# Kernel optimization log

Measured on AMD Instinct MI355X. Metric: run time of the kernel, lower is better.

The kernel has to match this reference:

```python
import jax, jax.numpy as jnp
import numpy as np

N_NODES = 50000
N_EDGES = 800000
IN_DIM = 128
HID_DIM = 128


def setup_inputs() -> dict:
    key = jax.random.key(0)
    k1, k2, k3, k4 = jax.random.split(key, 4)
    x = jax.random.normal(k1, (N_NODES, IN_DIM), dtype=jnp.float32)
    src = jax.random.randint(k2, (N_EDGES,), 0, N_NODES, dtype=jnp.int64)
    dst = jax.random.randint(k3, (N_EDGES,), 0, N_NODES, dtype=jnp.int64)
    W = jax.random.normal(k4, (IN_DIM, HID_DIM), dtype=jnp.float32) * (1.0 / np.sqrt(IN_DIM))
    b = jnp.zeros((HID_DIM,), dtype=jnp.float32)
    return {"x": x, "src": src, "dst": dst, "W": W, "b": b}


def reference(x, src, dst, W, b):
    # DGL GraphConv, norm='both': out = D_in^{-1/2} A D_out^{-1/2} x W + b
    n = x.shape[0]
    ones = jnp.ones((src.shape[0],), dtype=x.dtype)
    deg_out = jax.ops.segment_sum(ones, src, num_segments=n)  # out-degree of src side
    deg_in = jax.ops.segment_sum(ones, dst, num_segments=n)   # in-degree of dst side
    norm_src = jnp.clip(deg_out, 1.0, None) ** -0.5           # [N]
    norm_dst = jnp.clip(deg_in, 1.0, None) ** -0.5            # [N]
    h = x * norm_src[:, None]                                 # [N, in_dim]
    agg = jax.ops.segment_sum(h[src], dst, num_segments=n)    # SpMM: sum messages at dst
    agg = agg * norm_dst[:, None]
    return agg @ W + b
```

## Files before the change

### kernel.cpp

```cpp
#include <hip/hip_runtime.h>
#include <hip/hip_bf16.h>

#define DIM   128
#define BM    64
#define HALF_NODES 25088
#define HALF_PAIRS (HALF_NODES / 2)
#define FULL_PAIRS (2 * HALF_PAIRS)

typedef short  bf16x8 __attribute__((ext_vector_type(8)));
typedef float  f32x4  __attribute__((ext_vector_type(4)));

__device__ __forceinline__ ushort f2bf(float f) {
    uint u = __float_as_uint(f);
    return (ushort)((u + 0x7FFFu + ((u >> 16) & 1u)) >> 16);
}

__global__ __launch_bounds__(256) void cvtw_kernel(const float* __restrict__ W,
                                                   ushort* __restrict__ WT) {
    int idx = blockIdx.x * 256 + threadIdx.x;
    if (idx < DIM * DIM) {
        int k = idx >> 7, c = idx & 127;
        WT[c * DIM + k] = f2bf(W[idx]);
    }
}

__global__ __launch_bounds__(1024) void hist_kernel(const int* __restrict__ src,
                                                    const int* __restrict__ dst,
                                                    uint* __restrict__ histD,
                                                    uint* __restrict__ histS,
                                                    int* __restrict__ rank,
                                                    int n_edges, int pairs_row,
                                                    int nhalves, int chunk) {
    __shared__ uint h[FULL_PAIRS];
    const int c   = blockIdx.x;
    const int tid = threadIdx.x;
    const int beg = c * chunk;
    const int end = min(beg + chunk, n_edges);
    for (int pass = 0; pass < 2; ++pass) {
        const int* key = pass ? src : dst;
        uint* outb     = pass ? histS : histD;
        for (int hbase = 0; hbase < nhalves; hbase += 2) {
            const int plo    = hbase * HALF_PAIRS;
            const int wpairs = min(FULL_PAIRS, pairs_row - plo);
            const int wnodes = wpairs * 2;
            const int lo     = plo * 2;
            for (int j = tid; j < wpairs; j += 1024) h[j] = 0;
            __syncthreads();
            for (int e = beg + tid; e < end; e += 1024) {
                int r = key[e] - lo;
                if ((unsigned)r < (unsigned)wnodes) {
                    uint old = atomicAdd(&h[r >> 1], 1u << ((r & 1) * 16));
                    if (pass == 0)
                        rank[e] = (r & 1) ? (int)(old >> 16) : (int)(old & 0xFFFFu);
                }
            }
            __syncthreads();
            uint* row = outb + (size_t)c * pairs_row + plo;
            for (int j = tid; j < wpairs; j += 1024) row[j] = h[j];
            __syncthreads();
        }
    }
}

__global__ __launch_bounds__(256) void prefix_kernel(uint* __restrict__ histD,
                                                     uint* __restrict__ histS,
                                                     int* __restrict__ deg_in,
                                                     float* __restrict__ norm_src,
                                                     int pairs_row, int n_nodes,
                                                     int nchunk) {
    int id = blockIdx.x * 256 + threadIdx.x;
    bool isS = id >= pairs_row;
    int j = isS ? id - pairs_row : id;
    if (j >= pairs_row) return;
    uint* col = (isS ? histS : histD) + j;
    uint run0 = 0, run1 = 0;
    for (int c = 0; c < nchunk; ++c) {
        uint v = col[(size_t)c * pairs_row];
        col[(size_t)c * pairs_row] = run0 | (run1 << 16);
        run0 += v & 0xFFFFu;
        run1 += v >> 16;
    }
    int n0 = 2 * j, n1 = 2 * j + 1;
    if (isS) {
        if (n0 < n_nodes) norm_src[n0] = rsqrtf(fmaxf((float)run0, 1.0f));
        if (n1 < n_nodes) norm_src[n1] = rsqrtf(fmaxf((float)run1, 1.0f));
    } else {
        deg_in[n0] = (int)run0;
        deg_in[n1] = (int)run1;
    }
}

__global__ __launch_bounds__(1024) void scan4_kernel(const int* __restrict__ deg,
                                                     int* __restrict__ offs, int n) {
    __shared__ int w1[16], w2[16];
    const int tid = threadIdx.x, lane = tid & 63, wid = tid >> 6;
    const int base = blockIdx.x * 4096;

    int part = 0;
    for (int i = base ? tid : n; i < base; i += 1024) part += deg[i];
#pragma unroll
    for (int o = 32; o; o >>= 1) part += __shfl_xor(part, o);
    if (lane == 0) w1[wid] = part;
    __syncthreads();
    int prefix = 0;
#pragma unroll
    for (int k = 0; k < 16; ++k) prefix += w1[k];

    int i0 = base + tid * 4;
    int e0 = (i0 + 0 < n) ? deg[i0 + 0] : 0;
    int e1 = (i0 + 1 < n) ? deg[i0 + 1] : 0;
    int e2 = (i0 + 2 < n) ? deg[i0 + 2] : 0;
    int e3 = (i0 + 3 < n) ? deg[i0 + 3] : 0;
    int s  = e0 + e1 + e2 + e3;
    int sc = s;
#pragma unroll
    for (int o = 1; o < 64; o <<= 1) {
        int t = __shfl_up(sc, o);
        if (lane >= o) sc += t;
    }
    if (lane == 63) w2[wid] = sc;
    __syncthreads();
    int wpre = 0;
    for (int k = 0; k < wid; ++k) wpre += w2[k];
    int excl = prefix + wpre + sc - s;
    int o1 = excl + e0, o2 = o1 + e1, o3 = o2 + e2, o4 = o3 + e3;
    if (i0 + 0 < n) offs[i0 + 1] = o1;
    if (i0 + 1 < n) offs[i0 + 2] = o2;
    if (i0 + 2 < n) offs[i0 + 3] = o3;
    if (i0 + 3 < n) offs[i0 + 4] = o4;
    if (base == 0 && tid == 0) offs[0] = 0;
}

__global__ __launch_bounds__(256) void fill_kernel(const int* __restrict__ src,
                                                   const int* __restrict__ dst,
                                                   const int* __restrict__ offs,
                                                   const uint* __restrict__ histD,
                                                   const int* __restrict__ rank,
                                                   int* __restrict__ esrc,
                                                   int n_edges, int pairs_row,
                                                   int chunk) {
    int e = blockIdx.x * 256 + threadIdx.x;
    if (e >= n_edges) return;
    int t = dst[e];
    int c = e / chunk;
    uint pf = histD[(size_t)c * pairs_row + (t >> 1)];
    int pref = (t & 1) ? (int)(pf >> 16) : (int)(pf & 0xFFFFu);
    esrc[offs[t] + pref + rank[e]] = src[e];
}

__global__ __launch_bounds__(256, 4) void gemmx_kernel(const float* __restrict__ x,
                                                       const ushort* __restrict__ WT,
                                                       const float* __restrict__ norm_src,
                                                       ushort* __restrict__ h,
                                                       int n_nodes) {
    __shared__ ushort WsT[DIM * DIM];
    const int tid = threadIdx.x;

    {
        const uint4* wsrc = reinterpret_cast<const uint4*>(WT);
#pragma unroll
        for (int i = 0; i < 8; ++i) {
            int linear = tid + i * 256;
            uint4 v = wsrc[linear];
            int byte = linear * 16;
            int c = byte >> 8;
            int swz = byte ^ ((c & 7) << 4);
            *reinterpret_cast<uint4*>(reinterpret_cast<char*>(WsT) + swz) = v;
        }
    }
    __syncthreads();

    const int lane = tid & 63;
    const int w    = tid >> 6;
    const int r0   = blockIdx.x * BM;
    const int rowm = r0 + w * 16 + (lane & 15);
    const int rowc = min(rowm, n_nodes - 1);
    const float4* X4 = reinterpret_cast<const float4*>(x);

    f32x4 acc[8];
#pragma unroll
    for (int t = 0; t < 8; ++t) acc[t] = (f32x4){0.f, 0.f, 0.f, 0.f};

#pragma unroll
    for (int s = 0; s < 4; ++s) {
        int idx = rowc * 32 + s * 8 + (lane >> 4) * 2;
        float4 v0 = X4[idx];
        float4 v1 = X4[idx + 1];
        bf16x8 a;
        a[0] = (short)f2bf(v0.x); a[1] = (short)f2bf(v0.y);
        a[2] = (short)f2bf(v0.z); a[3] = (short)f2bf(v0.w);
        a[4] = (short)f2bf(v1.x); a[5] = (short)f2bf(v1.y);
        a[6] = (short)f2bf(v1.z); a[7] = (short)f2bf(v1.w);
#pragma unroll
        for (int t = 0; t < 8; ++t) {
            int c   = t * 16 + (lane & 15);
            int ofs = c * 256 + s * 64 + (lane >> 4) * 16;
            ofs ^= (c & 7) << 4;
            bf16x8 b = *reinterpret_cast<const bf16x8*>(
                reinterpret_cast<const char*>(WsT) + ofs);
            acc[t] = __builtin_amdgcn_mfma_f32_16x16x32_bf16(a, b, acc[t], 0, 0, 0);
        }
    }

#pragma unroll
    for (int i = 0; i < 4; ++i) {
        int row = r0 + w * 16 + (lane >> 4) * 4 + i;
        if (row < n_nodes) {
            float ns = norm_src[row];
            ushort* hp = h + (size_t)row * DIM + (lane & 15);
#pragma unroll
            for (int t = 0; t < 8; ++t)
                hp[t * 16] = f2bf(acc[t][i] * ns);
        }
    }
}

__global__ __launch_bounds__(256) void gather_kernel(const ushort* __restrict__ h,
                                                     const int* __restrict__ esrc,
                                                     const int* __restrict__ offs,
                                                     const float* __restrict__ bg,
                                                     float* __restrict__ out,
                                                     int n_nodes) {
    int node = blockIdx.x * 4 + (threadIdx.x >> 6);
    if (node >= n_nodes) return;
    int lane = threadIdx.x & 63;
    int j = offs[node], end = offs[node + 1];
    int deg = end - j;
    const uint* hp = reinterpret_cast<const uint*>(h);
    float ax[8], ay[8];
#pragma unroll
    for (int q = 0; q < 8; ++q) { ax[q] = 0.f; ay[q] = 0.f; }
    for (; j + 7 < end; j += 8) {
        int   si[8];
        uint  u[8];
#pragma unroll
        for (int q = 0; q < 8; ++q) si[q] = esrc[j + q];
#pragma unroll
        for (int q = 0; q < 8; ++q) u[q] = hp[(size_t)si[q] * 64 + lane];
#pragma unroll
        for (int q = 0; q < 8; ++q) {
            ax[q] += __uint_as_float(u[q] << 16);
            ay[q] += __uint_as_float(u[q] & 0xFFFF0000u);
        }
    }
    for (; j + 3 < end; j += 4) {
        int  si[4];
        uint u[4];
#pragma unroll
        for (int q = 0; q < 4; ++q) si[q] = esrc[j + q];
#pragma unroll
        for (int q = 0; q < 4; ++q) u[q] = hp[(size_t)si[q] * 64 + lane];
#pragma unroll
        for (int q = 0; q < 4; ++q) {
            ax[q] += __uint_as_float(u[q] << 16);
            ay[q] += __uint_as_float(u[q] & 0xFFFF0000u);
        }
    }
    for (; j < end; ++j) {
        uint u = hp[(size_t)esrc[j] * 64 + lane];
        ax[0] += __uint_as_float(u << 16);
        ay[0] += __uint_as_float(u & 0xFFFF0000u);
    }
    float sx = ((ax[0] + ax[1]) + (ax[2] + ax[3])) + ((ax[4] + ax[5]) + (ax[6] + ax[7]));
    float sy = ((ay[0] + ay[1]) + (ay[2] + ay[3])) + ((ay[4] + ay[5]) + (ay[6] + ay[7]));
    float nd = rsqrtf(fmaxf((float)deg, 1.0f));
    float2 bv = reinterpret_cast<const float2*>(bg)[lane];
    float2 r;
    r.x = sx * nd + bv.x;
    r.y = sy * nd + bv.y;
    reinterpret_cast<float2*>(out)[(size_t)node * 64 + lane] = r;
}

extern "C" void kernel_launch(void* const* d_in, const int* in_sizes, int n_in,
                              void* d_out, int out_size, void* d_ws, size_t ws_size,
                              hipStream_t stream) {
    const float* x   = (const float*)d_in[0];
    const int*   src = (const int*)d_in[1];
    const int*   dst = (const int*)d_in[2];
    const float* W   = (const float*)d_in[3];
    const float* b   = (const float*)d_in[4];
    float* out = (float*)d_out;

    const int n_nodes = in_sizes[0] / DIM;
    const int n_edges = in_sizes[1];

    const int nhalves   = (n_nodes + HALF_NODES - 1) / HALF_NODES;
    const int npad      = nhalves * HALF_NODES;
    const int pairs_row = npad / 2;

    auto need = [&](int C) -> size_t {
        return 2ull * n_nodes * DIM + 2ull * DIM * DIM +
               4ull * ((size_t)2 * npad + 1 + n_nodes +
                       2ull * C * pairs_row + 2ull * n_edges);
    };
    int C = 64;
    if (ws_size < need(64)) C = 32;
    if (ws_size < need(32)) C = 16;
    const int chunk = (n_edges + C - 1) / C;

    ushort* h        = (ushort*)d_ws;
    ushort* WT       = h + (size_t)n_nodes * DIM;
    int*    deg_in   = (int*)(WT + DIM * DIM);
    int*    offs     = deg_in + npad;
    float*  norm_src = (float*)(offs + npad + 1);
    uint*   histD    = (uint*)(norm_src + n_nodes);
    uint*   histS    = histD + (size_t)C * pairs_row;
    int*    rank     = (int*)(histS + (size_t)C * pairs_row);
    int*    esrc     = rank + n_edges;

    const int egrid = (n_edges + 255) / 256;

    cvtw_kernel<<<(DIM * DIM + 255) / 256, 256, 0, stream>>>(W, WT);
    hist_kernel<<<C, 1024, 0, stream>>>(src, dst, histD, histS, rank,
                                        n_edges, pairs_row, nhalves, chunk);
    prefix_kernel<<<(2 * pairs_row + 255) / 256, 256, 0, stream>>>(
        histD, histS, deg_in, norm_src, pairs_row, n_nodes, C);
    gemmx_kernel<<<(n_nodes + BM - 1) / BM, 256, 0, stream>>>(
        x, WT, norm_src, h, n_nodes);
    scan4_kernel<<<(npad + 4095) / 4096, 1024, 0, stream>>>(deg_in, offs, npad);
    fill_kernel<<<egrid, 256, 0, stream>>>(src, dst, offs, histD, rank, esrc,
                                           n_edges, pairs_row, chunk);
    gather_kernel<<<(n_nodes + 3) / 4, 256, 0, stream>>>(
        h, esrc, offs, b, out, n_nodes);
}
```

Measured before the change: 118.0 us.

## Fuse W conversion into prefix, halve gather wave per node, double hist chunks

Folds the W transpose/convert kernel into extra blocks of the prefix kernel, which removes one launch. The prefix kernel also skips writing back histS, since only histD's exclusive prefixes are used later. The gather now handles each node with 32 lanes loading 8 bytes each, so one block covers 8 nodes and uses wider float4 stores. The histogram chunk count rises to 128, giving more hist blocks for parallelism at the cost of a longer per-column prefix loop and more workspace.

```diff
diff --git a/kernel.cpp b/kernel.cpp
--- a/kernel.cpp
+++ b/kernel.cpp
@@ -13,15 +13,6 @@
 __device__ __forceinline__ ushort f2bf(float f) {
     uint u = __float_as_uint(f);
     return (ushort)((u + 0x7FFFu + ((u >> 16) & 1u)) >> 16);
-}
-
-__global__ __launch_bounds__(256) void cvtw_kernel(const float* __restrict__ W,
-                                                   ushort* __restrict__ WT) {
-    int idx = blockIdx.x * 256 + threadIdx.x;
-    if (idx < DIM * DIM) {
-        int k = idx >> 7, c = idx & 127;
-        WT[c * DIM + k] = f2bf(W[idx]);
-    }
 }
 
 __global__ __launch_bounds__(1024) void hist_kernel(const int* __restrict__ src,
@@ -63,30 +54,47 @@
 }
 
 __global__ __launch_bounds__(256) void prefix_kernel(uint* __restrict__ histD,
-                                                     uint* __restrict__ histS,
+                                                     const uint* __restrict__ histS,
                                                      int* __restrict__ deg_in,
                                                      float* __restrict__ norm_src,
+                                                     const float* __restrict__ W,
+                                                     ushort* __restrict__ WT,
                                                      int pairs_row, int n_nodes,
-                                                     int nchunk) {
+                                                     int nchunk, int nblk_main) {
+    if ((int)blockIdx.x >= nblk_main) {
+        int idx = ((int)blockIdx.x - nblk_main) * 256 + threadIdx.x;
+        if (idx < DIM * DIM) {
+            int k = idx >> 7, c = idx & 127;
+            WT[c * DIM + k] = f2bf(W[idx]);
+        }
+        return;
+    }
     int id = blockIdx.x * 256 + threadIdx.x;
     bool isS = id >= pairs_row;
     int j = isS ? id - pairs_row : id;
     if (j >= pairs_row) return;
-    uint* col = (isS ? histS : histD) + j;
-    uint run0 = 0, run1 = 0;
-    for (int c = 0; c < nchunk; ++c) {
-        uint v = col[(size_t)c * pairs_row];
-        col[(size_t)c * pairs_row] = run0 | (run1 << 16);
-        run0 += v & 0xFFFFu;
-        run1 += v >> 16;
-    }
-    int n0 = 2 * j, n1 = 2 * j + 1;
     if (isS) {
+        const uint* col = histS + j;
+        uint run0 = 0, run1 = 0;
+        for (int c = 0; c < nchunk; ++c) {
+            uint v = col[(size_t)c * pairs_row];
+            run0 += v & 0xFFFFu;
+            run1 += v >> 16;
+        }
+        int n0 = 2 * j, n1 = 2 * j + 1;
         if (n0 < n_nodes) norm_src[n0] = rsqrtf(fmaxf((float)run0, 1.0f));
         if (n1 < n_nodes) norm_src[n1] = rsqrtf(fmaxf((float)run1, 1.0f));
     } else {
-        deg_in[n0] = (int)run0;
-        deg_in[n1] = (int)run1;
+        uint* col = histD + j;
+        uint run0 = 0, run1 = 0;
+        for (int c = 0; c < nchunk; ++c) {
+            uint v = col[(size_t)c * pairs_row];
+            col[(size_t)c * pairs_row] = run0 | (run1 << 16);
+            run0 += v & 0xFFFFu;
+            run1 += v >> 16;
+        }
+        deg_in[2 * j]     = (int)run0;
+        deg_in[2 * j + 1] = (int)run1;
     }
 }
 
@@ -221,54 +229,54 @@
                                                      const float* __restrict__ bg,
                                                      float* __restrict__ out,
                                                      int n_nodes) {
-    int node = blockIdx.x * 4 + (threadIdx.x >> 6);
-    if (node >= n_nodes) return;
-    int lane = threadIdx.x & 63;
-    int j = offs[node], end = offs[node + 1];
-    int deg = end - j;
-    const uint* hp = reinterpret_cast<const uint*>(h);
-    float ax[8], ay[8];
-#pragma unroll
-    for (int q = 0; q < 8; ++q) { ax[q] = 0.f; ay[q] = 0.f; }
+    const int grp  = threadIdx.x >> 5;
+    const int node = blockIdx.x * 8 + grp;
+    const int l    = threadIdx.x & 31;
+    const bool valid = node < n_nodes;
+    int j = 0, end = 0;
+    if (valid) { j = offs[node]; end = offs[node + 1]; }
+    const int deg = end - j;
+    const uint2* hp = reinterpret_cast<const uint2*>(h);
+
+    float a[4][4];
+#pragma unroll
+    for (int q = 0; q < 4; ++q)
+#pragma unroll
+        for (int c = 0; c < 4; ++c) a[q][c] = 0.f;
+
     for (; j + 7 < end; j += 8) {
-        int   si[8];
-        uint  u[8];
-#pragma unroll
-        for (int q = 0; q < 8; ++q) si[q] = esrc[j + q];
-#pragma unroll
-        for (int q = 0; q < 8; ++q) u[q] = hp[(size_t)si[q] * 64 + lane];
+        int s[8];
+#pragma unroll
+        for (int q = 0; q < 8; ++q) s[q] = esrc[j + q];
+        uint2 u[8];
+#pragma unroll
+        for (int q = 0; q < 8; ++q) u[q] = hp[(size_t)s[q] * 32 + l];
 #pragma unroll
         for (int q = 0; q < 8; ++q) {
-            ax[q] += __uint_as_float(u[q] << 16);
-            ay[q] += __uint_as_float(u[q] & 0xFFFF0000u);
-        }
-    }
-    for (; j + 3 < end; j += 4) {
-        int  si[4];
-        uint u[4];
-#pragma unroll
-        for (int q = 0; q < 4; ++q) si[q] = esrc[j + q];
-#pragma unroll
-        for (int q = 0; q < 4; ++q) u[q] = hp[(size_t)si[q] * 64 + lane];
-#pragma unroll
-        for (int q = 0; q < 4; ++q) {
-            ax[q] += __uint_as_float(u[q] << 16);
-            ay[q] += __uint_as_float(u[q] & 0xFFFF0000u);
+            a[q & 3][0] += __uint_as_float(u[q].x << 16);
+            a[q & 3][1] += __uint_as_float(u[q].x & 0xFFFF0000u);
+            a[q & 3][2] += __uint_as_float(u[q].y << 16);
+            a[q & 3][3] += __uint_as_float(u[q].y & 0xFFFF0000u);
         }
     }
     for (; j < end; ++j) {
-        uint u = hp[(size_t)esrc[j] * 64 + lane];
-        ax[0] += __uint_as_float(u << 16);
-        ay[0] += __uint_as_float(u & 0xFFFF0000u);
-    }
-    float sx = ((ax[0] + ax[1]) + (ax[2] + ax[3])) + ((ax[4] + ax[5]) + (ax[6] + ax[7]));
-    float sy = ((ay[0] + ay[1]) + (ay[2] + ay[3])) + ((ay[4] + ay[5]) + (ay[6] + ay[7]));
-    float nd = rsqrtf(fmaxf((float)deg, 1.0f));
-    float2 bv = reinterpret_cast<const float2*>(bg)[lane];
-    float2 r;
-    r.x = sx * nd + bv.x;
-    r.y = sy * nd + bv.y;
-    reinterpret_cast<float2*>(out)[(size_t)node * 64 + lane] = r;
+        uint2 u = hp[(size_t)esrc[j] * 32 + l];
+        a[0][0] += __uint_as_float(u.x << 16);
+        a[0][1] += __uint_as_float(u.x & 0xFFFF0000u);
+        a[0][2] += __uint_as_float(u.y << 16);
+        a[0][3] += __uint_as_float(u.y & 0xFFFF0000u);
+    }
+
+    if (valid) {
+        float nd = rsqrtf(fmaxf((float)deg, 1.0f));
+        float4 bv = reinterpret_cast<const float4*>(bg)[l];
+        float4 r;
+        r.x = (a[0][0] + a[1][0] + a[2][0] + a[3][0]) * nd + bv.x;
+        r.y = (a[0][1] + a[1][1] + a[2][1] + a[3][1]) * nd + bv.y;
+        r.z = (a[0][2] + a[1][2] + a[2][2] + a[3][2]) * nd + bv.z;
+        r.w = (a[0][3] + a[1][3] + a[2][3] + a[3][3]) * nd + bv.w;
+        reinterpret_cast<float4*>(out)[(size_t)node * 32 + l] = r;
+    }
 }
 
 extern "C" void kernel_launch(void* const* d_in, const int* in_sizes, int n_in,
@@ -293,9 +301,9 @@
                4ull * ((size_t)2 * npad + 1 + n_nodes +
                        2ull * C * pairs_row + 2ull * n_edges);
     };
-    int C = 64;
-    if (ws_size < need(64)) C = 32;
-    if (ws_size < need(32)) C = 16;
+    int C = 128;
+    if (ws_size < need(128)) C = 64;
+    if (ws_size < need(64))  C = 32;
     const int chunk = (n_edges + C - 1) / C;
 
     ushort* h        = (ushort*)d_ws;
@@ -308,18 +316,18 @@
     int*    rank     = (int*)(histS + (size_t)C * pairs_row);
     int*    esrc     = rank + n_edges;
 
-    const int egrid = (n_edges + 255) / 256;
-
-    cvtw_kernel<<<(DIM * DIM + 255) / 256, 256, 0, stream>>>(W, WT);
+    const int egrid    = (n_edges + 255) / 256;
+    const int nblkpref = (2 * pairs_row + 255) / 256;
+
     hist_kernel<<<C, 1024, 0, stream>>>(src, dst, histD, histS, rank,
                                         n_edges, pairs_row, nhalves, chunk);
-    prefix_kernel<<<(2 * pairs_row + 255) / 256, 256, 0, stream>>>(
-        histD, histS, deg_in, norm_src, pairs_row, n_nodes, C);
+    prefix_kernel<<<nblkpref + (DIM * DIM + 255) / 256, 256, 0, stream>>>(
+        histD, histS, deg_in, norm_src, W, WT, pairs_row, n_nodes, C, nblkpref);
     gemmx_kernel<<<(n_nodes + BM - 1) / BM, 256, 0, stream>>>(
         x, WT, norm_src, h, n_nodes);
     scan4_kernel<<<(npad + 4095) / 4096, 1024, 0, stream>>>(deg_in, offs, npad);
     fill_kernel<<<egrid, 256, 0, stream>>>(src, dst, offs, histD, rank, esrc,
                                            n_edges, pairs_row, chunk);
-    gather_kernel<<<(n_nodes + 3) / 4, 256, 0, stream>>>(
+    gather_kernel<<<(n_nodes + 7) / 8, 256, 0, stream>>>(
         h, esrc, offs, b, out, n_nodes);
 }
```

Measured after the change: 128.9 us. +9.2%, slower.
